# Kernel optimization log

Hardware: AMD Instinct MI355X
Metric: run time of the kernel (lower is better)

Reference implementation:

```python
import jax, jax.numpy as jnp
import numpy as np

N, E = 50000, 800000
IN_DIM, HID, OUT_DIM, HEADS = 256, 128, 128, 2
EPS_BN = 1e-5


def _glorot(key, shape):
    fan_in, fan_out = shape[0], shape[-1]
    lim = float(np.sqrt(6.0 / (fan_in + fan_out)))
    return jax.random.uniform(key, shape, jnp.float32, -lim, lim)


def setup_inputs() -> dict:
    key = jax.random.key(0)
    ks = jax.random.split(key, 12)
    x = jax.random.normal(ks[0], (N, IN_DIM), jnp.float32)
    edge_index = jax.random.randint(ks[1], (2, E), 0, N, jnp.int64)
    return {
        "x": x,
        "edge_index": edge_index,
        # layer 1 (heads=2, concat)
        "W1": _glorot(ks[2], (IN_DIM, HEADS * HID)),
        "att_src1": _glorot(ks[3], (HEADS, HID)),
        "att_dst1": _glorot(ks[4], (HEADS, HID)),
        "b1": jnp.zeros((HEADS * HID,), jnp.float32),
        "g1": jnp.ones((HEADS * HID,), jnp.float32),
        "be1": jnp.zeros((HEADS * HID,), jnp.float32),
        # layer 2 (heads=1, no concat)
        "W2": _glorot(ks[5], (HEADS * HID, OUT_DIM)),
        "att_src2": _glorot(ks[6], (1, OUT_DIM)),
        "att_dst2": _glorot(ks[7], (1, OUT_DIM)),
        "b2": jnp.zeros((OUT_DIM,), jnp.float32),
        "g2": jnp.ones((OUT_DIM,), jnp.float32),
        "be2": jnp.zeros((OUT_DIM,), jnp.float32),
    }


def gat_conv(x, src, dst, W, att_src, att_dst, bias, heads, out_ch, concat):
    """PyG GATConv forward (dropout=identity at eval). Messages flow src->dst,
    softmax over incoming edges of dst, sum-aggregate."""
    h = (x @ W).reshape(-1, heads, out_ch)             # [N, H, C]
    a_s = jnp.einsum('nhc,hc->nh', h, att_src)          # [N, H]
    a_d = jnp.einsum('nhc,hc->nh', h, att_dst)
    e = jax.nn.leaky_relu(a_s[src] + a_d[dst], 0.2)     # [E, H]
    m = jax.ops.segment_max(e, dst, num_segments=N)     # [N, H]
    m = jnp.where(jnp.isfinite(m), m, 0.0)
    w = jnp.exp(e - m[dst])                             # [E, H]
    denom = jax.ops.segment_sum(w, dst, num_segments=N) # [N, H]
    alpha = w / (denom[dst] + 1e-16)                    # [E, H]
    msg = h[src] * alpha[:, :, None]                    # [E, H, C]
    out = jax.ops.segment_sum(msg, dst, num_segments=N) # [N, H, C]
    if concat:
        out = out.reshape(-1, heads * out_ch)
    else:
        out = out.mean(axis=1)
    return out + bias


def batchnorm_relu(x, gamma, beta):
    mu = x.mean(axis=0)
    var = x.var(axis=0)  # biased, as used for normalization in torch BN
    xn = (x - mu) * jax.lax.rsqrt(var + EPS_BN)
    return jax.nn.relu(xn * gamma + beta)


def reference(x, edge_index, W1, att_src1, att_dst1, b1, g1, be1,
              W2, att_src2, att_dst2, b2, g2, be2):
    src, dst = edge_index[0], edge_index[1]
    h = gat_conv(x, src, dst, W1, att_src1, att_dst1, b1, HEADS, HID, True)
    h = batchnorm_relu(h, g1, be1)
    h = gat_conv(h, src, dst, W2, att_src2, att_dst2, b2, 1, OUT_DIM, False)
    h = batchnorm_relu(h, g2, be2)
    return h
```

## Files before the change

kernel.cpp:

```cpp
#include <hip/hip_runtime.h>
#include <math.h>

#define IN_DIM 256
#define EPS_BN 1e-5f
#define NS 16

typedef __attribute__((ext_vector_type(8))) short short8v;
typedef __attribute__((ext_vector_type(4))) float f32x4;

__device__ __forceinline__ float lrelu(float v) { return v > 0.f ? v : 0.2f * v; }

__device__ __forceinline__ unsigned short f2bf(float f) {
    unsigned int u = __float_as_uint(f);
    u += 0x7fffu + ((u >> 16) & 1u);
    return (unsigned short)(u >> 16);
}
__device__ __forceinline__ float bf2f(unsigned short s) {
    return __uint_as_float((unsigned int)s << 16);
}

__device__ __forceinline__ void bfma(float2& a, unsigned int pw, float w) {
    a.x = fmaf(__uint_as_float(pw << 16), w, a.x);
    a.y = fmaf(__uint_as_float(pw & 0xffff0000u), w, a.y);
}

__device__ __forceinline__ void gld16(const void* g, void* l) {
    __builtin_amdgcn_global_load_lds((const __attribute__((address_space(1))) void*)g,
                                     (__attribute__((address_space(3))) void*)l, 16, 0, 0);
}

__device__ __forceinline__ int edge_at(const void* ei, int is64, long long i) {
    if (is64) return (int)((const long long*)ei)[i];
    return ((const int*)ei)[i];
}

__global__ __launch_bounds__(256) void prep_kernel(const float* __restrict__ x,
                                                   unsigned short* __restrict__ xb, long long n8,
                                                   const float* __restrict__ W1,
                                                   unsigned short* __restrict__ Wt1,
                                                   const float* __restrict__ W2,
                                                   unsigned short* __restrict__ Wt2,
                                                   const unsigned int* __restrict__ eiw,
                                                   int* __restrict__ flag, long long nwords) {
    __shared__ int nz;
    long long nbx = (n8 + 255) / 256;
    long long b = blockIdx.x;
    if (b < nbx) {
        long long i = b * 256 + threadIdx.x;
        if (i < n8) {
            const float4* p = (const float4*)(x + i * 8);
            float4 v0 = p[0], v1 = p[1];
            ushort4 o0, o1;
            o0.x = f2bf(v0.x); o0.y = f2bf(v0.y); o0.z = f2bf(v0.z); o0.w = f2bf(v0.w);
            o1.x = f2bf(v1.x); o1.y = f2bf(v1.y); o1.z = f2bf(v1.z); o1.w = f2bf(v1.w);
            *(ushort4*)(xb + i * 8) = o0;
            *(ushort4*)(xb + i * 8 + 4) = o1;
        }
        return;
    }
    b -= nbx;
    if (b < 256) {
        int idx = (int)b * 256 + threadIdx.x;
        int c = idx >> 8, k = idx & 255;
        Wt1[idx] = f2bf(W1[(long long)k * 256 + c]);
        return;
    }
    b -= 256;
    if (b < 128) {
        int idx = (int)b * 256 + threadIdx.x;
        int c = idx >> 8, k = idx & 255;
        Wt2[idx] = f2bf(W2[(long long)k * 128 + c]);
        return;
    }
    if (threadIdx.x == 0) nz = 0;
    __syncthreads();
    int cnt = 0;
    for (int i = 0; i < 4; i++) {
        long long idx = 2LL * (threadIdx.x + i * 256) + 1;
        if (idx < nwords && eiw[idx] != 0u) cnt++;
    }
    if (cnt) atomicAdd(&nz, 1);
    __syncthreads();
    if (threadIdx.x == 0) flag[0] = (nz == 0) ? 1 : 0;
}

__global__ void count_deg_kernel(const void* __restrict__ ei, const int* __restrict__ flag,
                                 int* __restrict__ deg, int E_) {
    int is64 = flag[0];
    int i = blockIdx.x * 256 + threadIdx.x;
    if (i < E_) {
        int d = edge_at(ei, is64, (long long)E_ + i);
        atomicAdd(&deg[d], 1);
    }
}

__global__ __launch_bounds__(256) void scan_partial_kernel(const int* __restrict__ deg,
                                                           int* __restrict__ bsum, int n) {
    __shared__ int sh[256];
    int t = threadIdx.x;
    int i = blockIdx.x * 256 + t;
    sh[t] = (i < n) ? deg[i] : 0;
    __syncthreads();
    for (int off = 128; off >= 1; off >>= 1) {
        if (t < off) sh[t] += sh[t + off];
        __syncthreads();
    }
    if (t == 0) bsum[blockIdx.x] = sh[0];
}

__global__ __launch_bounds__(256) void scan_write_kernel(const int* __restrict__ deg,
                                                         const int* __restrict__ bsum,
                                                         int* __restrict__ rowptr,
                                                         int* __restrict__ ctr, int n, int nb) {
    __shared__ int sh[256];
    __shared__ int base_sh;
    int t = threadIdx.x;
    int b = blockIdx.x;
    sh[t] = (t < b) ? bsum[t] : 0;
    __syncthreads();
    for (int off = 128; off >= 1; off >>= 1) {
        if (t < off) sh[t] += sh[t + off];
        __syncthreads();
    }
    if (t == 0) base_sh = sh[0];
    __syncthreads();
    int i = b * 256 + t;
    int d = (i < n) ? deg[i] : 0;
    sh[t] = d;
    __syncthreads();
    for (int off = 1; off < 256; off <<= 1) {
        int u = (t >= off) ? sh[t - off] : 0;
        __syncthreads();
        sh[t] += u;
        __syncthreads();
    }
    if (i < n) {
        int v = base_sh + sh[t] - d;
        rowptr[i] = v;
        ctr[i] = v;
    }
    if (b == nb - 1 && t == 255) rowptr[n] = base_sh + sh[255];
}

__global__ void scatter_kernel(const void* __restrict__ ei, const int* __restrict__ flag,
                               int* __restrict__ ctr, int* __restrict__ srcs, int E_) {
    int is64 = flag[0];
    int i = blockIdx.x * 256 + threadIdx.x;
    if (i < E_) {
        int s = edge_at(ei, is64, i);
        int d = edge_at(ei, is64, (long long)E_ + i);
        int pos = atomicAdd(&ctr[d], 1);
        srcs[pos] = s;
    }
}

template <int NCOL, int NH, bool FUSEBN>
__global__ __launch_bounds__(256) void gemm_mfma_kernel(const unsigned short* __restrict__ Ab,
                                                        const unsigned short* __restrict__ Wt,
                                                        unsigned short* __restrict__ C,
                                                        const float* __restrict__ att_s,
                                                        const float* __restrict__ att_d,
                                                        float* __restrict__ a_s,
                                                        float* __restrict__ a_d, int M,
                                                        const float* __restrict__ bnsh,
                                                        const float* __restrict__ gamma,
                                                        const float* __restrict__ beta) {
    __shared__ unsigned short B_lds[64 * 256];
    __shared__ unsigned short A_lds[128 * 64];
    __shared__ float scs[FUSEBN ? 256 : 1];
    __shared__ float shs[FUSEBN ? 256 : 1];
    const int t = threadIdx.x;
    const int w = t >> 6, l = t & 63;
    const int row0 = blockIdx.x * 128;
    const int col0 = blockIdx.y * 64;

    {
        const char* wb = (const char*)Wt + (size_t)col0 * 512;
#pragma unroll
        for (int it = 0; it < 8; ++it) {
            int q = w * 8 + it;
            int i = q * 64 + l;
            int r = i >> 5;
            int cs = (i & 31) ^ (r & 7);
            gld16(wb + (size_t)r * 512 + cs * 16, (char*)B_lds + q * 1024);
        }
    }

    short8v nxt[4];
    const char* ab = (const char*)Ab + (size_t)row0 * 512;

    if (FUSEBN) {
        {
            int c = t;
            float s = 0.f, q = 0.f;
#pragma unroll
            for (int sh = 0; sh < NS; sh++) { s += bnsh[sh * 512 + c]; q += bnsh[sh * 512 + 256 + c]; }
            float invN = 1.f / (float)M;
            float mu = s * invN;
            float var = q * invN - mu * mu;
            float sc = rsqrtf(var + EPS_BN) * gamma[c];
            scs[c] = sc;
            shs[c] = beta[c] - mu * sc;
        }
#pragma unroll
        for (int it = 0; it < 4; ++it) {
            int i = it * 256 + t;
            int r = i >> 3, g = i & 7;
            int gr = row0 + r;
            nxt[it] = (gr < M) ? *(const short8v*)(Ab + (size_t)gr * 256 + g * 8)
                               : (short8v)(short)0;
        }
        __syncthreads();
#pragma unroll
        for (int it = 0; it < 4; ++it) {
            int i = it * 256 + t;
            int r = i >> 3, g = i & 7;
            int kb = g * 8;
            float4 s0 = *(const float4*)&scs[kb], s1 = *(const float4*)&scs[kb + 4];
            float4 h0 = *(const float4*)&shs[kb], h1 = *(const float4*)&shs[kb + 4];
            short8v v = nxt[it];
            short8v ov;
            ov[0] = (short)f2bf(fmaxf(bf2f((unsigned short)v[0]) * s0.x + h0.x, 0.f));
            ov[1] = (short)f2bf(fmaxf(bf2f((unsigned short)v[1]) * s0.y + h0.y, 0.f));
            ov[2] = (short)f2bf(fmaxf(bf2f((unsigned short)v[2]) * s0.z + h0.z, 0.f));
            ov[3] = (short)f2bf(fmaxf(bf2f((unsigned short)v[3]) * s0.w + h0.w, 0.f));
            ov[4] = (short)f2bf(fmaxf(bf2f((unsigned short)v[4]) * s1.x + h1.x, 0.f));
            ov[5] = (short)f2bf(fmaxf(bf2f((unsigned short)v[5]) * s1.y + h1.y, 0.f));
            ov[6] = (short)f2bf(fmaxf(bf2f((unsigned short)v[6]) * s1.z + h1.z, 0.f));
            ov[7] = (short)f2bf(fmaxf(bf2f((unsigned short)v[7]) * s1.w + h1.w, 0.f));
            *(short8v*)((char*)A_lds + r * 128 + ((g ^ (r & 7)) << 4)) = ov;
        }
    } else {
#pragma unroll
        for (int it = 0; it < 4; ++it) {
            int q = w * 4 + it;
            int i = q * 64 + l;
            int r = i >> 3;
            int cs = (i & 7) ^ (r & 7);
            gld16(ab + (size_t)r * 512 + cs * 16, (char*)A_lds + q * 1024);
        }
    }
    __syncthreads();

    const int rl = l & 15, kg = l >> 4;
    f32x4 acc0[4], acc1[4];
#pragma unroll
    for (int i = 0; i < 4; ++i) { acc0[i] = (f32x4)(0.f); acc1[i] = (f32x4)(0.f); }

    const int ar0 = w * 32 + rl, ar1 = ar0 + 16;
    const int aswz = (ar0 & 7) << 4;

    for (int c = 0; c < 4; ++c) {
        if (FUSEBN && c < 3) {
#pragma unroll
            for (int it = 0; it < 4; ++it) {
                int i = it * 256 + t;
                int r = i >> 3, g = i & 7;
                int gr = row0 + r;
                nxt[it] = (gr < M) ? *(const short8v*)(Ab + (size_t)gr * 256 + (c + 1) * 64 + g * 8)
                                   : (short8v)(short)0;
            }
        }
#pragma unroll
        for (int s = 0; s < 2; ++s) {
            short8v a0 = *(const short8v*)((const char*)A_lds +
                          ((ar0 * 128 + s * 64 + kg * 16) ^ aswz));
            short8v a1 = *(const short8v*)((const char*)A_lds +
                          ((ar1 * 128 + s * 64 + kg * 16) ^ aswz));
#pragma unroll
            for (int ct = 0; ct < 4; ++ct) {
                int br = ct * 16 + rl;
                short8v bfr = *(const short8v*)((const char*)B_lds +
                               ((br * 512 + c * 128 + s * 64 + kg * 16) ^ ((br & 7) << 4)));
                acc0[ct] = __builtin_amdgcn_mfma_f32_16x16x32_bf16(a0, bfr, acc0[ct], 0, 0, 0);
                acc1[ct] = __builtin_amdgcn_mfma_f32_16x16x32_bf16(a1, bfr, acc1[ct], 0, 0, 0);
            }
        }
        __syncthreads();
        if (c < 3) {
            if (FUSEBN) {
#pragma unroll
                for (int it = 0; it < 4; ++it) {
                    int i = it * 256 + t;
                    int r = i >> 3, g = i & 7;
                    int kb = (c + 1) * 64 + g * 8;
                    float4 s0 = *(const float4*)&scs[kb], s1 = *(const float4*)&scs[kb + 4];
                    float4 h0 = *(const float4*)&shs[kb], h1 = *(const float4*)&shs[kb + 4];
                    short8v v = nxt[it];
                    short8v ov;
                    ov[0] = (short)f2bf(fmaxf(bf2f((unsigned short)v[0]) * s0.x + h0.x, 0.f));
                    ov[1] = (short)f2bf(fmaxf(bf2f((unsigned short)v[1]) * s0.y + h0.y, 0.f));
                    ov[2] = (short)f2bf(fmaxf(bf2f((unsigned short)v[2]) * s0.z + h0.z, 0.f));
                    ov[3] = (short)f2bf(fmaxf(bf2f((unsigned short)v[3]) * s0.w + h0.w, 0.f));
                    ov[4] = (short)f2bf(fmaxf(bf2f((unsigned short)v[4]) * s1.x + h1.x, 0.f));
                    ov[5] = (short)f2bf(fmaxf(bf2f((unsigned short)v[5]) * s1.y + h1.y, 0.f));
                    ov[6] = (short)f2bf(fmaxf(bf2f((unsigned short)v[6]) * s1.z + h1.z, 0.f));
                    ov[7] = (short)f2bf(fmaxf(bf2f((unsigned short)v[7]) * s1.w + h1.w, 0.f));
                    *(short8v*)((char*)A_lds + r * 128 + ((g ^ (r & 7)) << 4)) = ov;
                }
            } else {
#pragma unroll
                for (int it = 0; it < 4; ++it) {
                    int q = w * 4 + it;
                    int i = q * 64 + l;
                    int r = i >> 3;
                    int cs = (i & 7) ^ (r & 7);
                    gld16(ab + (size_t)r * 512 + (c + 1) * 128 + cs * 16, (char*)A_lds + q * 1024);
                }
            }
            __syncthreads();
        }
    }

#pragma unroll
    for (int ct = 0; ct < 4; ++ct) {
#pragma unroll
        for (int r = 0; r < 4; ++r) {
            int gr0 = row0 + w * 32 + kg * 4 + r;
            if (gr0 < M) C[(long long)gr0 * NCOL + col0 + ct * 16 + rl] = f2bf(acc0[ct][r]);
            int gr1 = gr0 + 16;
            if (gr1 < M) C[(long long)gr1 * NCOL + col0 + ct * 16 + rl] = f2bf(acc1[ct][r]);
        }
    }

    float asp0[4] = {}, adp0[4] = {}, asp1[4] = {}, adp1[4] = {};
#pragma unroll
    for (int ct = 0; ct < 4; ++ct) {
        int col = col0 + ct * 16 + rl;
        float vs = att_s[col], vd = att_d[col];
#pragma unroll
        for (int r = 0; r < 4; ++r) {
            asp0[r] += acc0[ct][r] * vs; adp0[r] += acc0[ct][r] * vd;
            asp1[r] += acc1[ct][r] * vs; adp1[r] += acc1[ct][r] * vd;
        }
    }
#pragma unroll
    for (int off = 1; off < 16; off <<= 1) {
#pragma unroll
        for (int r = 0; r < 4; ++r) {
            asp0[r] += __shfl_xor(asp0[r], off);
            adp0[r] += __shfl_xor(adp0[r], off);
            asp1[r] += __shfl_xor(asp1[r], off);
            adp1[r] += __shfl_xor(adp1[r], off);
        }
    }
    if (rl == 0) {
        int head = (NH == 2) ? (col0 >> 7) : 0;
#pragma unroll
        for (int r = 0; r < 4; ++r) {
            int gr0 = row0 + w * 32 + kg * 4 + r;
            if (gr0 < M) {
                atomicAdd(&a_s[gr0 * NH + head], asp0[r]);
                atomicAdd(&a_d[gr0 * NH + head], adp0[r]);
            }
            int gr1 = gr0 + 16;
            if (gr1 < M) {
                atomicAdd(&a_s[gr1 * NH + head], asp1[r]);
                atomicAdd(&a_d[gr1 * NH + head], adp1[r]);
            }
        }
    }
}

__global__ __launch_bounds__(256) void aggregate1_kernel(const unsigned short* __restrict__ h,
                                                         const int* __restrict__ rowptr,
                                                         const int* __restrict__ srcs,
                                                         const float* __restrict__ a_s,
                                                         const float* __restrict__ a_d,
                                                         const float* __restrict__ bias,
                                                         unsigned short* __restrict__ out,
                                                         float* __restrict__ bnsh, int Nn) {
    __shared__ float sw_lds[4][256];
    const int t = threadIdx.x;
    const int wid = t >> 6, lane = t & 63;
    const int hh = (lane >> 4) & 1;
    const int eb = lane >> 5;
    const int colb = (lane & 31) * 8;
    float* wbase = sw_lds[wid];
    float2 bnsum2[4] = {}, bnsq2[4] = {};
    const int stride = gridDim.x * 4;

    for (int n = blockIdx.x * 4 + wid; n < Nn; n += stride) {
        int beg = rowptr[n], end = rowptr[n + 1];
        float2 adv = *(const float2*)&a_d[(size_t)n * 2];
        float ad0 = adv.x, ad1 = adv.y;
        float2 acc2[4] = {};
        float den = 0.f, m0 = -1e30f, m1 = -1e30f;

        for (int cb = beg; cb < end; cb += 64) {
            int cnt = end - cb; if (cnt > 64) cnt = 64;
            float e0 = -1e30f, e1 = -1e30f;
            int s_l = 0;
            if (lane < cnt) {
                s_l = srcs[cb + lane];
                float2 av = *(const float2*)&a_s[(size_t)s_l * 2];
                e0 = lrelu(av.x + ad0);
                e1 = lrelu(av.y + ad1);
            }
            float cm0 = e0, cm1 = e1;
            for (int off = 32; off >= 1; off >>= 1) {
                cm0 = fmaxf(cm0, __shfl_xor(cm0, off));
                cm1 = fmaxf(cm1, __shfl_xor(cm1, off));
            }
            if (cm0 > m0 || cm1 > m1) {
                float f0 = (cm0 > m0) ? __expf(m0 - cm0) : 1.f;
                float f1 = (cm1 > m1) ? __expf(m1 - cm1) : 1.f;
                m0 = fmaxf(m0, cm0); m1 = fmaxf(m1, cm1);
                float fo = hh ? f1 : f0;
#pragma unroll
                for (int j = 0; j < 4; j++) { acc2[j].x *= fo; acc2[j].y *= fo; }
                den *= fo;
            }
            if (lane < cnt) {
                *(float2*)&wbase[lane * 2] = make_float2(__int_as_float(s_l), __expf(e0 - m0));
                *(float2*)&wbase[128 + lane * 2] = make_float2(__int_as_float(s_l), __expf(e1 - m1));
            }
            int c = 0;
            for (; c + 8 <= cnt; c += 8) {
                float2 sw0 = *(const float2*)&wbase[hh * 128 + (c + eb) * 2];
                float2 sw1 = *(const float2*)&wbase[hh * 128 + (c + 2 + eb) * 2];
                float2 sw2 = *(const float2*)&wbase[hh * 128 + (c + 4 + eb) * 2];
                float2 sw3 = *(const float2*)&wbase[hh * 128 + (c + 6 + eb) * 2];
                uint4 p0 = *(const uint4*)(h + ((size_t)__float_as_int(sw0.x) << 8) + colb);
                uint4 p1 = *(const uint4*)(h + ((size_t)__float_as_int(sw1.x) << 8) + colb);
                uint4 p2 = *(const uint4*)(h + ((size_t)__float_as_int(sw2.x) << 8) + colb);
                uint4 p3 = *(const uint4*)(h + ((size_t)__float_as_int(sw3.x) << 8) + colb);
                den += sw0.y + sw1.y + sw2.y + sw3.y;
                bfma(acc2[0], p0.x, sw0.y); bfma(acc2[1], p0.y, sw0.y);
                bfma(acc2[2], p0.z, sw0.y); bfma(acc2[3], p0.w, sw0.y);
                bfma(acc2[0], p1.x, sw1.y); bfma(acc2[1], p1.y, sw1.y);
                bfma(acc2[2], p1.z, sw1.y); bfma(acc2[3], p1.w, sw1.y);
                bfma(acc2[0], p2.x, sw2.y); bfma(acc2[1], p2.y, sw2.y);
                bfma(acc2[2], p2.z, sw2.y); bfma(acc2[3], p2.w, sw2.y);
                bfma(acc2[0], p3.x, sw3.y); bfma(acc2[1], p3.y, sw3.y);
                bfma(acc2[2], p3.z, sw3.y); bfma(acc2[3], p3.w, sw3.y);
            }
            for (; c + 4 <= cnt; c += 4) {
                float2 sw0 = *(const float2*)&wbase[hh * 128 + (c + eb) * 2];
                float2 sw1 = *(const float2*)&wbase[hh * 128 + (c + 2 + eb) * 2];
                uint4 p0 = *(const uint4*)(h + ((size_t)__float_as_int(sw0.x) << 8) + colb);
                uint4 p1 = *(const uint4*)(h + ((size_t)__float_as_int(sw1.x) << 8) + colb);
                den += sw0.y + sw1.y;
                bfma(acc2[0], p0.x, sw0.y); bfma(acc2[1], p0.y, sw0.y);
                bfma(acc2[2], p0.z, sw0.y); bfma(acc2[3], p0.w, sw0.y);
// ... 175 lines not shown
            for (int j = 0; j < 4; j++) {
                bnsum2[j].x += of[2 * j];     bnsum2[j].y += of[2 * j + 1];
                bnsq2[j].x += of[2 * j] * of[2 * j];
                bnsq2[j].y += of[2 * j + 1] * of[2 * j + 1];
            }
            float* ob = out + (size_t)n * 128 + colb;
            *(float4*)ob = make_float4(of[0], of[1], of[2], of[3]);
            *(float4*)(ob + 4) = make_float4(of[4], of[5], of[6], of[7]);
        }
    }

    __syncthreads();
    if (lane < 16) {
#pragma unroll
        for (int j = 0; j < 4; j++) {
            wbase[colb + 2 * j] = bnsum2[j].x;
            wbase[colb + 2 * j + 1] = bnsum2[j].y;
        }
    }
    __syncthreads();
    if (t < 128) {
        int sh = (blockIdx.x & (NS - 1)) * 256;
        float s = sw_lds[0][t] + sw_lds[1][t] + sw_lds[2][t] + sw_lds[3][t];
        atomicAdd(&bnsh[sh + t], s);
    }
    __syncthreads();
    if (lane < 16) {
#pragma unroll
        for (int j = 0; j < 4; j++) {
            wbase[colb + 2 * j] = bnsq2[j].x;
            wbase[colb + 2 * j + 1] = bnsq2[j].y;
        }
    }
    __syncthreads();
    if (t < 128) {
        int sh = (blockIdx.x & (NS - 1)) * 256;
        float q = sw_lds[0][t] + sw_lds[1][t] + sw_lds[2][t] + sw_lds[3][t];
        atomicAdd(&bnsh[sh + 128 + t], q);
    }
}

__global__ __launch_bounds__(256) void bn_apply_final_kernel(float* __restrict__ x,
                                                             const float* __restrict__ bnsh,
                                                             const float* __restrict__ gamma,
                                                             const float* __restrict__ beta,
                                                             int Nn) {
    int t = threadIdx.x;
    int col = t & 127;
    float s = 0.f, q = 0.f;
#pragma unroll
    for (int sh = 0; sh < NS; sh++) { s += bnsh[sh * 256 + col]; q += bnsh[sh * 256 + 128 + col]; }
    float mu = s / (float)Nn;
    float var = q / (float)Nn - mu * mu;
    float sc = rsqrtf(var + EPS_BN) * gamma[col];
    float sh_ = beta[col] - mu * sc;
    int r0 = blockIdx.x * 2 + (t >> 7);
    int rs = gridDim.x * 2;
    for (int r = r0; r < Nn; r += rs) {
        size_t idx = (size_t)r * 128 + col;
        x[idx] = fmaxf(x[idx] * sc + sh_, 0.f);
    }
}

extern "C" void kernel_launch(void* const* d_in, const int* in_sizes, int n_in,
                              void* d_out, int out_size, void* d_ws, size_t ws_size,
                              hipStream_t stream) {
    const float* x        = (const float*)d_in[0];
    const void*  ei       = d_in[1];
    const float* W1       = (const float*)d_in[2];
    const float* att_src1 = (const float*)d_in[3];
    const float* att_dst1 = (const float*)d_in[4];
    const float* b1       = (const float*)d_in[5];
    const float* g1       = (const float*)d_in[6];
    const float* be1      = (const float*)d_in[7];
    const float* W2       = (const float*)d_in[8];
    const float* att_src2 = (const float*)d_in[9];
    const float* att_dst2 = (const float*)d_in[10];
    const float* b2       = (const float*)d_in[11];
    const float* g2       = (const float*)d_in[12];
    const float* be2      = (const float*)d_in[13];

    const int Nn = in_sizes[0] / IN_DIM;
    const int E_ = in_sizes[1] / 2;
    const int gb = (Nn + 127) / 128;
    const int Mpad = gb * 128 + 128;

    char* ws = (char*)d_ws;
    size_t o = 0;
    auto alloc = [&](size_t bytes) {
        size_t r = o;
        o += (bytes + 255) & ~(size_t)255;
        return r;
    };
    int* flag = (int*)(ws + alloc(4));
    size_t z0 = o;
    int*   deg   = (int*)(ws + alloc((size_t)Nn * 4));
    float* as1   = (float*)(ws + alloc((size_t)Nn * 2 * 4));
    float* ad1   = (float*)(ws + alloc((size_t)Nn * 2 * 4));
    float* as2   = (float*)(ws + alloc((size_t)Nn * 4));
    float* ad2   = (float*)(ws + alloc((size_t)Nn * 4));
    float* bn1sh = (float*)(ws + alloc((size_t)NS * 512 * 4));
    float* bn2sh = (float*)(ws + alloc((size_t)NS * 256 * 4));
    size_t z1 = o;
    int*   rowptr = (int*)(ws + alloc((size_t)(Nn + 1) * 4));
    int*   ctr    = (int*)(ws + alloc((size_t)Nn * 4));
    int*   srcs   = (int*)(ws + alloc((size_t)E_ * 4));
    int*   bsum   = (int*)(ws + alloc(256 * 4));
    unsigned short* Wt1  = (unsigned short*)(ws + alloc((size_t)256 * 256 * 2));
    unsigned short* Wt2  = (unsigned short*)(ws + alloc((size_t)128 * 256 * 2));
    unsigned short* xb   = (unsigned short*)(ws + alloc((size_t)Mpad * 256 * 2));
    unsigned short* x2b0 = (unsigned short*)(ws + alloc((size_t)Nn * 256 * 2));
    unsigned short* h1b  = (unsigned short*)(ws + alloc((size_t)Nn * 256 * 2));
    unsigned short* h2b  = (unsigned short*)(ws + alloc((size_t)Nn * 128 * 2));
    float* outf = (float*)d_out;

    hipMemsetAsync(ws + z0, 0, z1 - z0, stream);

    {
        long long n8 = (long long)Nn * 256 / 8;
        long long grid = (n8 + 255) / 256 + 256 + 128 + 1;
        prep_kernel<<<(int)grid, 256, 0, stream>>>(x, xb, n8, W1, Wt1, W2, Wt2,
                                                   (const unsigned int*)ei, flag,
                                                   (long long)2 * E_);
    }

    int eb = (E_ + 255) / 256;
    int nsb = (Nn + 255) / 256;
    count_deg_kernel<<<eb, 256, 0, stream>>>(ei, flag, deg, E_);
    scan_partial_kernel<<<nsb, 256, 0, stream>>>(deg, bsum, Nn);
    scan_write_kernel<<<nsb, 256, 0, stream>>>(deg, bsum, rowptr, ctr, Nn, nsb);
    scatter_kernel<<<eb, 256, 0, stream>>>(ei, flag, ctr, srcs, E_);

    const int agg_blocks = 2048;

    gemm_mfma_kernel<256, 2, false><<<dim3(gb, 4), 256, 0, stream>>>(
        xb, Wt1, h1b, att_src1, att_dst1, as1, ad1, Nn, nullptr, nullptr, nullptr);
    aggregate1_kernel<<<agg_blocks, 256, 0, stream>>>(h1b, rowptr, srcs, as1, ad1, b1, x2b0,
                                                      bn1sh, Nn);

    gemm_mfma_kernel<128, 1, true><<<dim3(gb, 2), 256, 0, stream>>>(
        x2b0, Wt2, h2b, att_src2, att_dst2, as2, ad2, Nn, bn1sh, g1, be1);
    aggregate2_kernel<<<agg_blocks, 256, 0, stream>>>(h2b, rowptr, srcs, as2, ad2, b2, outf,
                                                      bn2sh, Nn);
    bn_apply_final_kernel<<<512, 256, 0, stream>>>(outf, bn2sh, g2, be2, Nn);
}
```

Baseline: 293.6 us.

## Fuse fp32-to-bf16 input conversion into GEMM1 and restructure GEMMs over full K rows

GEMM1 now reads fp32 x directly and converts it to bf16 in LDS, which removes the separate conversion pass and the xb buffer. Both GEMMs switch to 64-row blocks that keep the full 256-wide A tile resident and loop over output column panels, so A is loaded and BN-transformed once per block rather than once per column block. The two-kernel scan is merged into one kernel in which each block re-sums all preceding degrees, saving a launch at the cost of quadratic redundant reads. The column loop within a block is now serialized, and the 64 KB of LDS per block may reduce occupancy.

```diff
diff --git a/kernel.cpp b/kernel.cpp
--- a/kernel.cpp
+++ b/kernel.cpp
@@ -34,31 +34,14 @@
     return ((const int*)ei)[i];
 }
 
-__global__ __launch_bounds__(256) void prep_kernel(const float* __restrict__ x,
-                                                   unsigned short* __restrict__ xb, long long n8,
-                                                   const float* __restrict__ W1,
+__global__ __launch_bounds__(256) void prep_kernel(const float* __restrict__ W1,
                                                    unsigned short* __restrict__ Wt1,
                                                    const float* __restrict__ W2,
                                                    unsigned short* __restrict__ Wt2,
                                                    const unsigned int* __restrict__ eiw,
                                                    int* __restrict__ flag, long long nwords) {
     __shared__ int nz;
-    long long nbx = (n8 + 255) / 256;
     long long b = blockIdx.x;
-    if (b < nbx) {
-        long long i = b * 256 + threadIdx.x;
-        if (i < n8) {
-            const float4* p = (const float4*)(x + i * 8);
-            float4 v0 = p[0], v1 = p[1];
-            ushort4 o0, o1;
-            o0.x = f2bf(v0.x); o0.y = f2bf(v0.y); o0.z = f2bf(v0.z); o0.w = f2bf(v0.w);
-            o1.x = f2bf(v1.x); o1.y = f2bf(v1.y); o1.z = f2bf(v1.z); o1.w = f2bf(v1.w);
-            *(ushort4*)(xb + i * 8) = o0;
-            *(ushort4*)(xb + i * 8 + 4) = o1;
-        }
-        return;
-    }
-    b -= nbx;
     if (b < 256) {
         int idx = (int)b * 256 + threadIdx.x;
         int c = idx >> 8, k = idx & 255;
@@ -94,29 +77,17 @@
     }
 }
 
-__global__ __launch_bounds__(256) void scan_partial_kernel(const int* __restrict__ deg,
-                                                           int* __restrict__ bsum, int n) {
-    __shared__ int sh[256];
-    int t = threadIdx.x;
-    int i = blockIdx.x * 256 + t;
-    sh[t] = (i < n) ? deg[i] : 0;
-    __syncthreads();
-    for (int off = 128; off >= 1; off >>= 1) {
-        if (t < off) sh[t] += sh[t + off];
-        __syncthreads();
-    }
-    if (t == 0) bsum[blockIdx.x] = sh[0];
-}
-
-__global__ __launch_bounds__(256) void scan_write_kernel(const int* __restrict__ deg,
-                                                         const int* __restrict__ bsum,
-                                                         int* __restrict__ rowptr,
-                                                         int* __restrict__ ctr, int n, int nb) {
+__global__ __launch_bounds__(256) void scan_kernel(const int* __restrict__ deg,
+                                                   int* __restrict__ rowptr,
+                                                   int* __restrict__ ctr, int n, int nb) {
     __shared__ int sh[256];
     __shared__ int base_sh;
     int t = threadIdx.x;
     int b = blockIdx.x;
-    sh[t] = (t < b) ? bsum[t] : 0;
+    int lim = b * 256;
+    int s = 0;
+    for (int j = t; j < lim; j += 256) s += deg[j];
+    sh[t] = s;
     __syncthreads();
     for (int off = 128; off >= 1; off >>= 1) {
         if (t < off) sh[t] += sh[t + off];
@@ -124,7 +95,7 @@
     }
     if (t == 0) base_sh = sh[0];
     __syncthreads();
-    int i = b * 256 + t;
+    int i = lim + t;
     int d = (i < n) ? deg[i] : 0;
     sh[t] = d;
     __syncthreads();
@@ -154,209 +125,228 @@
     }
 }
 
-template <int NCOL, int NH, bool FUSEBN>
-__global__ __launch_bounds__(256) void gemm_mfma_kernel(const unsigned short* __restrict__ Ab,
-                                                        const unsigned short* __restrict__ Wt,
-                                                        unsigned short* __restrict__ C,
-                                                        const float* __restrict__ att_s,
-                                                        const float* __restrict__ att_d,
-                                                        float* __restrict__ a_s,
-                                                        float* __restrict__ a_d, int M,
-                                                        const float* __restrict__ bnsh,
-                                                        const float* __restrict__ gamma,
-                                                        const float* __restrict__ beta) {
-    __shared__ unsigned short B_lds[64 * 256];
-    __shared__ unsigned short A_lds[128 * 64];
-    __shared__ float scs[FUSEBN ? 256 : 1];
-    __shared__ float shs[FUSEBN ? 256 : 1];
+__global__ __launch_bounds__(256) void gemm1_kernel(const float* __restrict__ X,
+                                                    const unsigned short* __restrict__ Wt,
+                                                    unsigned short* __restrict__ C,
+                                                    const float* __restrict__ att_s,
+                                                    const float* __restrict__ att_d,
+                                                    float* __restrict__ a_s,
+                                                    float* __restrict__ a_d, int M) {
+    __shared__ __attribute__((aligned(16))) unsigned short A_lds[64 * 256];
+    __shared__ __attribute__((aligned(16))) unsigned short B_lds[64 * 256];
     const int t = threadIdx.x;
     const int w = t >> 6, l = t & 63;
-    const int row0 = blockIdx.x * 128;
-    const int col0 = blockIdx.y * 64;
-
-    {
-        const char* wb = (const char*)Wt + (size_t)col0 * 512;
-#pragma unroll
-        for (int it = 0; it < 8; ++it) {
-            int q = w * 8 + it;
-            int i = q * 64 + l;
-            int r = i >> 5;
-            int cs = (i & 31) ^ (r & 7);
-            gld16(wb + (size_t)r * 512 + cs * 16, (char*)B_lds + q * 1024);
-        }
-    }
-
-    short8v nxt[4];
-    const char* ab = (const char*)Ab + (size_t)row0 * 512;
-
-    if (FUSEBN) {
+    const int row0 = blockIdx.x * 64;
+    const int g = t & 31;
+
+#pragma unroll
+    for (int it = 0; it < 8; ++it) {
+        int i = it * 256 + t;
+        int r = i >> 5;
+        int gr = row0 + r;
+        float4 v0 = make_float4(0.f, 0.f, 0.f, 0.f), v1 = v0;
+        if (gr < M) {
+            const float* src = X + (size_t)gr * 256 + g * 8;
+            v0 = *(const float4*)src;
+            v1 = *(const float4*)(src + 4);
+        }
+        short8v ov;
+        ov[0] = (short)f2bf(v0.x); ov[1] = (short)f2bf(v0.y);
+        ov[2] = (short)f2bf(v0.z); ov[3] = (short)f2bf(v0.w);
+        ov[4] = (short)f2bf(v1.x); ov[5] = (short)f2bf(v1.y);
+        ov[6] = (short)f2bf(v1.z); ov[7] = (short)f2bf(v1.w);
+        *(short8v*)((char*)A_lds + r * 512 + ((g ^ (r & 7)) << 4)) = ov;
+    }
+
+    const int rl = l & 15, kg = l >> 4;
+    const int abase = (w * 16 + rl) * 512;
+    const int aswz = (w * 16 + rl) & 7;
+
+    float asp[4] = {}, adp[4] = {};
+    for (int p = 0; p < 4; ++p) {
+        __syncthreads();
         {
-            int c = t;
-            float s = 0.f, q = 0.f;
-#pragma unroll
-            for (int sh = 0; sh < NS; sh++) { s += bnsh[sh * 512 + c]; q += bnsh[sh * 512 + 256 + c]; }
-            float invN = 1.f / (float)M;
-            float mu = s * invN;
-            float var = q * invN - mu * mu;
-            float sc = rsqrtf(var + EPS_BN) * gamma[c];
-            scs[c] = sc;
-            shs[c] = beta[c] - mu * sc;
-        }
-#pragma unroll
-        for (int it = 0; it < 4; ++it) {
-            int i = it * 256 + t;
-            int r = i >> 3, g = i & 7;
-            int gr = row0 + r;
-            nxt[it] = (gr < M) ? *(const short8v*)(Ab + (size_t)gr * 256 + g * 8)
-                               : (short8v)(short)0;
+            const char* wb = (const char*)Wt + (size_t)(p * 64) * 512;
+#pragma unroll
+            for (int it = 0; it < 8; ++it) {
+                int q = w * 8 + it;
+                int i = q * 64 + l;
+                int r = i >> 5;
+                int cs = (i & 31) ^ (r & 7);
+                gld16(wb + (size_t)r * 512 + cs * 16, (char*)B_lds + q * 1024);
+            }
         }
         __syncthreads();
-#pragma unroll
-        for (int it = 0; it < 4; ++it) {
-            int i = it * 256 + t;
-            int r = i >> 3, g = i & 7;
-            int kb = g * 8;
-            float4 s0 = *(const float4*)&scs[kb], s1 = *(const float4*)&scs[kb + 4];
-            float4 h0 = *(const float4*)&shs[kb], h1 = *(const float4*)&shs[kb + 4];
-            short8v v = nxt[it];
-            short8v ov;
-            ov[0] = (short)f2bf(fmaxf(bf2f((unsigned short)v[0]) * s0.x + h0.x, 0.f));
-            ov[1] = (short)f2bf(fmaxf(bf2f((unsigned short)v[1]) * s0.y + h0.y, 0.f));
-            ov[2] = (short)f2bf(fmaxf(bf2f((unsigned short)v[2]) * s0.z + h0.z, 0.f));
-            ov[3] = (short)f2bf(fmaxf(bf2f((unsigned short)v[3]) * s0.w + h0.w, 0.f));
-            ov[4] = (short)f2bf(fmaxf(bf2f((unsigned short)v[4]) * s1.x + h1.x, 0.f));
-            ov[5] = (short)f2bf(fmaxf(bf2f((unsigned short)v[5]) * s1.y + h1.y, 0.f));
-            ov[6] = (short)f2bf(fmaxf(bf2f((unsigned short)v[6]) * s1.z + h1.z, 0.f));
-            ov[7] = (short)f2bf(fmaxf(bf2f((unsigned short)v[7]) * s1.w + h1.w, 0.f));
-            *(short8v*)((char*)A_lds + r * 128 + ((g ^ (r & 7)) << 4)) = ov;
-        }
-    } else {
-#pragma unroll
-        for (int it = 0; it < 4; ++it) {
-            int q = w * 4 + it;
-            int i = q * 64 + l;
-            int r = i >> 3;
-            int cs = (i & 7) ^ (r & 7);
-            gld16(ab + (size_t)r * 512 + cs * 16, (char*)A_lds + q * 1024);
-        }
-    }
-    __syncthreads();
-
-    const int rl = l & 15, kg = l >> 4;
-    f32x4 acc0[4], acc1[4];
-#pragma unroll
-    for (int i = 0; i < 4; ++i) { acc0[i] = (f32x4)(0.f); acc1[i] = (f32x4)(0.f); }
-
-    const int ar0 = w * 32 + rl, ar1 = ar0 + 16;
-    const int aswz = (ar0 & 7) << 4;
-
-    for (int c = 0; c < 4; ++c) {
-        if (FUSEBN && c < 3) {
-#pragma unroll
-            for (int it = 0; it < 4; ++it) {
-                int i = it * 256 + t;
-                int r = i >> 3, g = i & 7;
-                int gr = row0 + r;
-                nxt[it] = (gr < M) ? *(const short8v*)(Ab + (size_t)gr * 256 + (c + 1) * 64 + g * 8)
-                                   : (short8v)(short)0;
-            }
-        }
-#pragma unroll
-        for (int s = 0; s < 2; ++s) {
-            short8v a0 = *(const short8v*)((const char*)A_lds +
-                          ((ar0 * 128 + s * 64 + kg * 16) ^ aswz));
-            short8v a1 = *(const short8v*)((const char*)A_lds +
-                          ((ar1 * 128 + s * 64 + kg * 16) ^ aswz));
+        f32x4 acc[4];
+#pragma unroll
+        for (int i = 0; i < 4; ++i) acc[i] = (f32x4)(0.f);
+#pragma unroll
+        for (int ks = 0; ks < 8; ++ks) {
+            int chunk = ks * 4 + kg;
+            short8v a = *(const short8v*)((const char*)A_lds + abase + ((chunk ^ aswz) << 4));
 #pragma unroll
             for (int ct = 0; ct < 4; ++ct) {
                 int br = ct * 16 + rl;
-                short8v bfr = *(const short8v*)((const char*)B_lds +
-                               ((br * 512 + c * 128 + s * 64 + kg * 16) ^ ((br & 7) << 4)));
-                acc0[ct] = __builtin_amdgcn_mfma_f32_16x16x32_bf16(a0, bfr, acc0[ct], 0, 0, 0);
-                acc1[ct] = __builtin_amdgcn_mfma_f32_16x16x32_bf16(a1, bfr, acc1[ct], 0, 0, 0);
-            }
-        }
+                short8v b = *(const short8v*)((const char*)B_lds + br * 512 +
+                                              ((chunk ^ (br & 7)) << 4));
+                acc[ct] = __builtin_amdgcn_mfma_f32_16x16x32_bf16(a, b, acc[ct], 0, 0, 0);
+            }
+        }
+#pragma unroll
+        for (int ct = 0; ct < 4; ++ct) {
+            int col = p * 64 + ct * 16 + rl;
+            float vs = att_s[col], vd = att_d[col];
+#pragma unroll
+            for (int r = 0; r < 4; ++r) {
+                int gr = row0 + w * 16 + kg * 4 + r;
+                if (gr < M) C[(size_t)gr * 256 + col] = f2bf(acc[ct][r]);
+                asp[r] += acc[ct][r] * vs;
+                adp[r] += acc[ct][r] * vd;
+            }
+        }
+        if (p == 1 || p == 3) {
+            int head = p >> 1;
+#pragma unroll
+            for (int off = 1; off < 16; off <<= 1) {
+#pragma unroll
+                for (int r = 0; r < 4; ++r) {
+                    asp[r] += __shfl_xor(asp[r], off);
+                    adp[r] += __shfl_xor(adp[r], off);
+                }
+            }
+            if (rl == 0) {
+#pragma unroll
+                for (int r = 0; r < 4; ++r) {
+                    int gr = row0 + w * 16 + kg * 4 + r;
+                    if (gr < M) {
+                        atomicAdd(&a_s[gr * 2 + head], asp[r]);
+                        atomicAdd(&a_d[gr * 2 + head], adp[r]);
+                    }
+                }
+            }
+#pragma unroll
+            for (int r = 0; r < 4; ++r) { asp[r] = 0.f; adp[r] = 0.f; }
+        }
+    }
+}
+
+__global__ __launch_bounds__(256) void gemm2_kernel(const unsigned short* __restrict__ Ab,
+                                                    const unsigned short* __restrict__ Wt,
+                                                    unsigned short* __restrict__ C,
+                                                    const float* __restrict__ att_s,
+                                                    const float* __restrict__ att_d,
+                                                    float* __restrict__ a_s,
+                                                    float* __restrict__ a_d, int M,
+                                                    const float* __restrict__ bnsh,
+                                                    const float* __restrict__ gamma,
+                                                    const float* __restrict__ beta) {
+    __shared__ __attribute__((aligned(16))) unsigned short A_lds[64 * 256];
+    __shared__ __attribute__((aligned(16))) unsigned short B_lds[64 * 256];
+    const int t = threadIdx.x;
+    const int w = t >> 6, l = t & 63;
+    const int row0 = blockIdx.x * 64;
+    const int g = t & 31;
+
+    {
+        float* cf = (float*)A_lds;
+        float s = 0.f, q = 0.f;
+#pragma unroll
+        for (int sh = 0; sh < NS; sh++) { s += bnsh[sh * 512 + t]; q += bnsh[sh * 512 + 256 + t]; }
+        float invN = 1.f / (float)M;
+        float mu = s * invN;
+        float var = q * invN - mu * mu;
+        float scl = rsqrtf(var + EPS_BN) * gamma[t];
+        cf[t] = scl;
+        cf[256 + t] = beta[t] - mu * scl;
+    }
+    __syncthreads();
+    float sc[8], sb[8];
+    {
+        const float* cf = (const float*)A_lds;
+#pragma unroll
+        for (int j = 0; j < 8; ++j) {
+            sc[j] = cf[g * 8 + j];
+            sb[j] = cf[256 + g * 8 + j];
+        }
+    }
+    __syncthreads();
+
+#pragma unroll
+    for (int it = 0; it < 8; ++it) {
+        int i = it * 256 + t;
+        int r = i >> 5;
+        int gr = row0 + r;
+        short8v v = (gr < M) ? *(const short8v*)(Ab + (size_t)gr * 256 + g * 8)
+                             : (short8v)(short)0;
+        short8v ov;
+#pragma unroll
+        for (int j = 0; j < 8; ++j)
+            ov[j] = (short)f2bf(fmaxf(bf2f((unsigned short)v[j]) * sc[j] + sb[j], 0.f));
+        *(short8v*)((char*)A_lds + r * 512 + ((g ^ (r & 7)) << 4)) = ov;
+    }
+
+    const int rl = l & 15, kg = l >> 4;
+    const int abase = (w * 16 + rl) * 512;
+    const int aswz = (w * 16 + rl) & 7;
+
+    float asp[4] = {}, adp[4] = {};
+    for (int p = 0; p < 2; ++p) {
         __syncthreads();
-        if (c < 3) {
-            if (FUSEBN) {
-#pragma unroll
-                for (int it = 0; it < 4; ++it) {
-                    int i = it * 256 + t;
-                    int r = i >> 3, g = i & 7;
-                    int kb = (c + 1) * 64 + g * 8;
-                    float4 s0 = *(const float4*)&scs[kb], s1 = *(const float4*)&scs[kb + 4];
-                    float4 h0 = *(const float4*)&shs[kb], h1 = *(const float4*)&shs[kb + 4];
-                    short8v v = nxt[it];
-                    short8v ov;
-                    ov[0] = (short)f2bf(fmaxf(bf2f((unsigned short)v[0]) * s0.x + h0.x, 0.f));
-                    ov[1] = (short)f2bf(fmaxf(bf2f((unsigned short)v[1]) * s0.y + h0.y, 0.f));
-                    ov[2] = (short)f2bf(fmaxf(bf2f((unsigned short)v[2]) * s0.z + h0.z, 0.f));
-                    ov[3] = (short)f2bf(fmaxf(bf2f((unsigned short)v[3]) * s0.w + h0.w, 0.f));
-                    ov[4] = (short)f2bf(fmaxf(bf2f((unsigned short)v[4]) * s1.x + h1.x, 0.f));
-                    ov[5] = (short)f2bf(fmaxf(bf2f((unsigned short)v[5]) * s1.y + h1.y, 0.f));
-                    ov[6] = (short)f2bf(fmaxf(bf2f((unsigned short)v[6]) * s1.z + h1.z, 0.f));
-                    ov[7] = (short)f2bf(fmaxf(bf2f((unsigned short)v[7]) * s1.w + h1.w, 0.f));
-                    *(short8v*)((char*)A_lds + r * 128 + ((g ^ (r & 7)) << 4)) = ov;
-                }
-            } else {
-#pragma unroll
-                for (int it = 0; it < 4; ++it) {
-                    int q = w * 4 + it;
-                    int i = q * 64 + l;
-                    int r = i >> 3;
-                    int cs = (i & 7) ^ (r & 7);
-                    gld16(ab + (size_t)r * 512 + (c + 1) * 128 + cs * 16, (char*)A_lds + q * 1024);
-                }
-            }
-            __syncthreads();
-        }
-    }
-
-#pragma unroll
-    for (int ct = 0; ct < 4; ++ct) {
+        {
+            const char* wb = (const char*)Wt + (size_t)(p * 64) * 512;
+#pragma unroll
+            for (int it = 0; it < 8; ++it) {
+                int q = w * 8 + it;
+                int i = q * 64 + l;
+                int r = i >> 5;
+                int cs = (i & 31) ^ (r & 7);
+                gld16(wb + (size_t)r * 512 + cs * 16, (char*)B_lds + q * 1024);
+            }
+        }
+        __syncthreads();
+        f32x4 acc[4];
+#pragma unroll
+        for (int i = 0; i < 4; ++i) acc[i] = (f32x4)(0.f);
+#pragma unroll
+        for (int ks = 0; ks < 8; ++ks) {
+            int chunk = ks * 4 + kg;
+            short8v a = *(const short8v*)((const char*)A_lds + abase + ((chunk ^ aswz) << 4));
+#pragma unroll
+            for (int ct = 0; ct < 4; ++ct) {
+                int br = ct * 16 + rl;
+                short8v b = *(const short8v*)((const char*)B_lds + br * 512 +
+                                              ((chunk ^ (br & 7)) << 4));
+                acc[ct] = __builtin_amdgcn_mfma_f32_16x16x32_bf16(a, b, acc[ct], 0, 0, 0);
+            }
+        }
+#pragma unroll
+        for (int ct = 0; ct < 4; ++ct) {
+            int col = p * 64 + ct * 16 + rl;
+            float vs = att_s[col], vd = att_d[col];
+#pragma unroll
+            for (int r = 0; r < 4; ++r) {
+                int gr = row0 + w * 16 + kg * 4 + r;
+                if (gr < M) C[(size_t)gr * 128 + col] = f2bf(acc[ct][r]);
+                asp[r] += acc[ct][r] * vs;
+                adp[r] += acc[ct][r] * vd;
+            }
+        }
+    }
+#pragma unroll
+    for (int off = 1; off < 16; off <<= 1) {
 #pragma unroll
         for (int r = 0; r < 4; ++r) {
-            int gr0 = row0 + w * 32 + kg * 4 + r;
-            if (gr0 < M) C[(long long)gr0 * NCOL + col0 + ct * 16 + rl] = f2bf(acc0[ct][r]);
-            int gr1 = gr0 + 16;
-            if (gr1 < M) C[(long long)gr1 * NCOL + col0 + ct * 16 + rl] = f2bf(acc1[ct][r]);
-        }
-    }
-
-    float asp0[4] = {}, adp0[4] = {}, asp1[4] = {}, adp1[4] = {};
-#pragma unroll
-    for (int ct = 0; ct < 4; ++ct) {
-        int col = col0 + ct * 16 + rl;
-        float vs = att_s[col], vd = att_d[col];
+            asp[r] += __shfl_xor(asp[r], off);
+            adp[r] += __shfl_xor(adp[r], off);
+        }
+    }
+    if (rl == 0) {
 #pragma unroll
         for (int r = 0; r < 4; ++r) {
-            asp0[r] += acc0[ct][r] * vs; adp0[r] += acc0[ct][r] * vd;
-            asp1[r] += acc1[ct][r] * vs; adp1[r] += acc1[ct][r] * vd;
-        }
-    }
-#pragma unroll
-    for (int off = 1; off < 16; off <<= 1) {
-#pragma unroll
-        for (int r = 0; r < 4; ++r) {
-            asp0[r] += __shfl_xor(asp0[r], off);
-            adp0[r] += __shfl_xor(adp0[r], off);
-            asp1[r] += __shfl_xor(asp1[r], off);
-            adp1[r] += __shfl_xor(adp1[r], off);
-        }
-    }
-    if (rl == 0) {
-        int head = (NH == 2) ? (col0 >> 7) : 0;
-#pragma unroll
-        for (int r = 0; r < 4; ++r) {
-            int gr0 = row0 + w * 32 + kg * 4 + r;
-            if (gr0 < M) {
-                atomicAdd(&a_s[gr0 * NH + head], asp0[r]);
-                atomicAdd(&a_d[gr0 * NH + head], adp0[r]);
-            }
-            int gr1 = gr0 + 16;
-            if (gr1 < M) {
-                atomicAdd(&a_s[gr1 * NH + head], asp1[r]);
-                atomicAdd(&a_d[gr1 * NH + head], adp1[r]);
+            int gr = row0 + w * 16 + kg * 4 + r;
+            if (gr < M) {
+                atomicAdd(&a_s[gr], asp[r]);
+                atomicAdd(&a_d[gr], adp[r]);
             }
         }
     }
@@ -701,8 +691,7 @@
 
     const int Nn = in_sizes[0] / IN_DIM;
     const int E_ = in_sizes[1] / 2;
-    const int gb = (Nn + 127) / 128;
-    const int Mpad = gb * 128 + 128;
+    const int gb64 = (Nn + 63) / 64;
 
     char* ws = (char*)d_ws;
     size_t o = 0;
@@ -724,10 +713,8 @@
     int*   rowptr = (int*)(ws + alloc((size_t)(Nn + 1) * 4));
     int*   ctr    = (int*)(ws + alloc((size_t)Nn * 4));
     int*   srcs   = (int*)(ws + alloc((size_t)E_ * 4));
-    int*   bsum   = (int*)(ws + alloc(256 * 4));
     unsigned short* Wt1  = (unsigned short*)(ws + alloc((size_t)256 * 256 * 2));
     unsigned short* Wt2  = (unsigned short*)(ws + alloc((size_t)128 * 256 * 2));
-    unsigned short* xb   = (unsigned short*)(ws + alloc((size_t)Mpad * 256 * 2));
     unsigned short* x2b0 = (unsigned short*)(ws + alloc((size_t)Nn * 256 * 2));
     unsigned short* h1b  = (unsigned short*)(ws + alloc((size_t)Nn * 256 * 2));
     unsigned short* h2b  = (unsigned short*)(ws + alloc((size_t)Nn * 128 * 2));
@@ -735,30 +722,24 @@
 
     hipMemsetAsync(ws + z0, 0, z1 - z0, stream);
 
-    {
-        long long n8 = (long long)Nn * 256 / 8;
-        long long grid = (n8 + 255) / 256 + 256 + 128 + 1;
-        prep_kernel<<<(int)grid, 256, 0, stream>>>(x, xb, n8, W1, Wt1, W2, Wt2,
+    prep_kernel<<<256 + 128 + 1, 256, 0, stream>>>(W1, Wt1, W2, Wt2,
                                                    (const unsigned int*)ei, flag,
                                                    (long long)2 * E_);
-    }
 
     int eb = (E_ + 255) / 256;
     int nsb = (Nn + 255) / 256;
     count_deg_kernel<<<eb, 256, 0, stream>>>(ei, flag, deg, E_);
-    scan_partial_kernel<<<nsb, 256, 0, stream>>>(deg, bsum, Nn);
-    scan_write_kernel<<<nsb, 256, 0, stream>>>(deg, bsum, rowptr, ctr, Nn, nsb);
+    scan_kernel<<<nsb, 256, 0, stream>>>(deg, rowptr, ctr, Nn, nsb);
     scatter_kernel<<<eb, 256, 0, stream>>>(ei, flag, ctr, srcs, E_);
 
     const int agg_blocks = 2048;
 
-    gemm_mfma_kernel<256, 2, false><<<dim3(gb, 4), 256, 0, stream>>>(
-        xb, Wt1, h1b, att_src1, att_dst1, as1, ad1, Nn, nullptr, nullptr, nullptr);
+    gemm1_kernel<<<gb64, 256, 0, stream>>>(x, Wt1, h1b, att_src1, att_dst1, as1, ad1, Nn);
     aggregate1_kernel<<<agg_blocks, 256, 0, stream>>>(h1b, rowptr, srcs, as1, ad1, b1, x2b0,
                                                       bn1sh, Nn);
 
-    gemm_mfma_kernel<128, 1, true><<<dim3(gb, 2), 256, 0, stream>>>(
-        x2b0, Wt2, h2b, att_src2, att_dst2, as2, ad2, Nn, bn1sh, g1, be1);
+    gemm2_kernel<<<gb64, 256, 0, stream>>>(x2b0, Wt2, h2b, att_src2, att_dst2, as2, ad2, Nn,
+                                           bn1sh, g1, be1);
     aggregate2_kernel<<<agg_blocks, 256, 0, stream>>>(h2b, rowptr, srcs, as2, ad2, b2, outf,
                                                       bn2sh, Nn);
     bn_apply_final_kernel<<<512, 256, 0, stream>>>(outf, bn2sh, g2, be2, Nn);
```

New measurement: 307.7 us. 1.05x slower.

## Merge preprocessing launches: fold degree count, single-pass scan, scatter with GEMM1

Applied to the files above, without the earlier changes.

Removes the separate flag computation by having each wavefront detect int64 edge indices with a ballot. The degree count is folded into the prep kernel, and the two-pass scan becomes one kernel in which each block re-sums all preceding degrees. The edge scatter runs in the same launch as the first-layer GEMM, so the two can overlap. This cuts kernel launches and serialization gaps, at the cost of redundant prefix summation and redundant per-wave dtype checks. The GEMM body is turned into a shared device function.

```diff
diff --git a/kernel.cpp b/kernel.cpp
--- a/kernel.cpp
+++ b/kernel.cpp
@@ -34,15 +34,23 @@
     return ((const int*)ei)[i];
 }
 
-__global__ __launch_bounds__(256) void prep_kernel(const float* __restrict__ x,
-                                                   unsigned short* __restrict__ xb, long long n8,
-                                                   const float* __restrict__ W1,
-                                                   unsigned short* __restrict__ Wt1,
-                                                   const float* __restrict__ W2,
-                                                   unsigned short* __restrict__ Wt2,
-                                                   const unsigned int* __restrict__ eiw,
-                                                   int* __restrict__ flag, long long nwords) {
-    __shared__ int nz;
+__device__ __forceinline__ int edge_is64(const void* ei, int E_) {
+    const unsigned int* w = (const unsigned int*)ei;
+    int lane = threadIdx.x & 63;
+    long long idx = 2LL * lane + 1;
+    unsigned int v = (idx < 2LL * E_) ? w[idx] : 0u;
+    return (__ballot(v != 0u) == 0ULL) ? 1 : 0;
+}
+
+__global__ __launch_bounds__(256) void prep_count_kernel(const float* __restrict__ x,
+                                                         unsigned short* __restrict__ xb,
+                                                         long long n8,
+                                                         const float* __restrict__ W1,
+                                                         unsigned short* __restrict__ Wt1,
+                                                         const float* __restrict__ W2,
+                                                         unsigned short* __restrict__ Wt2,
+                                                         const void* __restrict__ ei,
+                                                         int* __restrict__ deg, int E_) {
     long long nbx = (n8 + 255) / 256;
     long long b = blockIdx.x;
     if (b < nbx) {
@@ -72,51 +80,26 @@
         Wt2[idx] = f2bf(W2[(long long)k * 128 + c]);
         return;
     }
-    if (threadIdx.x == 0) nz = 0;
-    __syncthreads();
-    int cnt = 0;
-    for (int i = 0; i < 4; i++) {
-        long long idx = 2LL * (threadIdx.x + i * 256) + 1;
-        if (idx < nwords && eiw[idx] != 0u) cnt++;
-    }
-    if (cnt) atomicAdd(&nz, 1);
-    __syncthreads();
-    if (threadIdx.x == 0) flag[0] = (nz == 0) ? 1 : 0;
-}
-
-__global__ void count_deg_kernel(const void* __restrict__ ei, const int* __restrict__ flag,
-                                 int* __restrict__ deg, int E_) {
-    int is64 = flag[0];
-    int i = blockIdx.x * 256 + threadIdx.x;
+    b -= 128;
+    int is64 = edge_is64(ei, E_);
+    int i = (int)b * 256 + threadIdx.x;
     if (i < E_) {
         int d = edge_at(ei, is64, (long long)E_ + i);
         atomicAdd(&deg[d], 1);
     }
 }
 
-__global__ __launch_bounds__(256) void scan_partial_kernel(const int* __restrict__ deg,
-                                                           int* __restrict__ bsum, int n) {
-    __shared__ int sh[256];
-    int t = threadIdx.x;
-    int i = blockIdx.x * 256 + t;
-    sh[t] = (i < n) ? deg[i] : 0;
-    __syncthreads();
-    for (int off = 128; off >= 1; off >>= 1) {
-        if (t < off) sh[t] += sh[t + off];
-        __syncthreads();
-    }
-    if (t == 0) bsum[blockIdx.x] = sh[0];
-}
-
-__global__ __launch_bounds__(256) void scan_write_kernel(const int* __restrict__ deg,
-                                                         const int* __restrict__ bsum,
-                                                         int* __restrict__ rowptr,
-                                                         int* __restrict__ ctr, int n, int nb) {
+__global__ __launch_bounds__(256) void scan_kernel(const int* __restrict__ deg,
+                                                   int* __restrict__ rowptr,
+                                                   int* __restrict__ ctr, int n, int nb) {
     __shared__ int sh[256];
     __shared__ int base_sh;
     int t = threadIdx.x;
     int b = blockIdx.x;
-    sh[t] = (t < b) ? bsum[t] : 0;
+    int lim = b * 256;
+    int s = 0;
+    for (int j = t; j < lim; j += 256) s += deg[j];
+    sh[t] = s;
     __syncthreads();
     for (int off = 128; off >= 1; off >>= 1) {
         if (t < off) sh[t] += sh[t + off];
@@ -124,7 +107,7 @@
     }
     if (t == 0) base_sh = sh[0];
     __syncthreads();
-    int i = b * 256 + t;
+    int i = lim + t;
     int d = (i < n) ? deg[i] : 0;
     sh[t] = d;
     __syncthreads();
@@ -142,37 +125,22 @@
     if (b == nb - 1 && t == 255) rowptr[n] = base_sh + sh[255];
 }
 
-__global__ void scatter_kernel(const void* __restrict__ ei, const int* __restrict__ flag,
-                               int* __restrict__ ctr, int* __restrict__ srcs, int E_) {
-    int is64 = flag[0];
-    int i = blockIdx.x * 256 + threadIdx.x;
-    if (i < E_) {
-        int s = edge_at(ei, is64, i);
-        int d = edge_at(ei, is64, (long long)E_ + i);
-        int pos = atomicAdd(&ctr[d], 1);
-        srcs[pos] = s;
-    }
-}
-
 template <int NCOL, int NH, bool FUSEBN>
-__global__ __launch_bounds__(256) void gemm_mfma_kernel(const unsigned short* __restrict__ Ab,
-                                                        const unsigned short* __restrict__ Wt,
-                                                        unsigned short* __restrict__ C,
-                                                        const float* __restrict__ att_s,
-                                                        const float* __restrict__ att_d,
-                                                        float* __restrict__ a_s,
-                                                        float* __restrict__ a_d, int M,
-                                                        const float* __restrict__ bnsh,
-                                                        const float* __restrict__ gamma,
-                                                        const float* __restrict__ beta) {
-    __shared__ unsigned short B_lds[64 * 256];
-    __shared__ unsigned short A_lds[128 * 64];
-    __shared__ float scs[FUSEBN ? 256 : 1];
-    __shared__ float shs[FUSEBN ? 256 : 1];
+__device__ __forceinline__ void gemm_body(unsigned short* A_lds, unsigned short* B_lds,
+                                          float* scs, float* shs,
+                                          const unsigned short* __restrict__ Ab,
+                                          const unsigned short* __restrict__ Wt,
+                                          unsigned short* __restrict__ C,
+                                          const float* __restrict__ att_s,
+                                          const float* __restrict__ att_d,
+                                          float* __restrict__ a_s,
+                                          float* __restrict__ a_d, int M,
+                                          int row0, int col0,
+                                          const float* __restrict__ bnsh,
+                                          const float* __restrict__ gamma,
+                                          const float* __restrict__ beta) {
     const int t = threadIdx.x;
     const int w = t >> 6, l = t & 63;
-    const int row0 = blockIdx.x * 128;
-    const int col0 = blockIdx.y * 64;
 
     {
         const char* wb = (const char*)Wt + (size_t)col0 * 512;
@@ -360,6 +328,57 @@
             }
         }
     }
+}
+
+__global__ __launch_bounds__(256) void scatter_gemm1_kernel(const void* __restrict__ ei,
+                                                            int* __restrict__ ctr,
+                                                            int* __restrict__ srcs, int E_,
+                                                            int eb, int gbx,
+                                                            const unsigned short* __restrict__ xb,
+                                                            const unsigned short* __restrict__ Wt1,
+                                                            unsigned short* __restrict__ h1b,
+                                                            const float* __restrict__ att_s,
+                                                            const float* __restrict__ att_d,
+                                                            float* __restrict__ a_s,
+                                                            float* __restrict__ a_d, int M) {
+    __shared__ __attribute__((aligned(16))) unsigned short B_lds[64 * 256];
+    __shared__ __attribute__((aligned(16))) unsigned short A_lds[128 * 64];
+    int b = blockIdx.x;
+    if (b < eb) {
+        int is64 = edge_is64(ei, E_);
+        int i = b * 256 + threadIdx.x;
+        if (i < E_) {
+            int s = edge_at(ei, is64, i);
+            int d = edge_at(ei, is64, (long long)E_ + i);
+            int pos = atomicAdd(&ctr[d], 1);
+            srcs[pos] = s;
+        }
+        return;
+    }
+    b -= eb;
+    int bx = b % gbx;
+    int by = b / gbx;
+    gemm_body<256, 2, false>(A_lds, B_lds, (float*)A_lds, (float*)A_lds, xb, Wt1, h1b,
+                             att_s, att_d, a_s, a_d, M, bx * 128, by * 64,
+                             nullptr, nullptr, nullptr);
+}
+
+__global__ __launch_bounds__(256) void gemm2_kernel(const unsigned short* __restrict__ Ab,
+                                                    const unsigned short* __restrict__ Wt,
+                                                    unsigned short* __restrict__ C,
+                                                    const float* __restrict__ att_s,
+                                                    const float* __restrict__ att_d,
+                                                    float* __restrict__ a_s,
+                                                    float* __restrict__ a_d, int M,
+                                                    const float* __restrict__ bnsh,
+                                                    const float* __restrict__ gamma,
+                                                    const float* __restrict__ beta) {
+    __shared__ __attribute__((aligned(16))) unsigned short B_lds[64 * 256];
+    __shared__ __attribute__((aligned(16))) unsigned short A_lds[128 * 64];
+    __shared__ float scs[256];
+    __shared__ float shs[256];
+    gemm_body<128, 1, true>(A_lds, B_lds, scs, shs, Ab, Wt, C, att_s, att_d, a_s, a_d,
+                            M, blockIdx.x * 128, blockIdx.y * 64, bnsh, gamma, beta);
 }
 
 __global__ __launch_bounds__(256) void aggregate1_kernel(const unsigned short* __restrict__ h,
@@ -711,7 +730,6 @@
         o += (bytes + 255) & ~(size_t)255;
         return r;
     };
-    int* flag = (int*)(ws + alloc(4));
     size_t z0 = o;
     int*   deg   = (int*)(ws + alloc((size_t)Nn * 4));
     float* as1   = (float*)(ws + alloc((size_t)Nn * 2 * 4));
@@ -724,7 +742,6 @@
     int*   rowptr = (int*)(ws + alloc((size_t)(Nn + 1) * 4));
     int*   ctr    = (int*)(ws + alloc((size_t)Nn * 4));
     int*   srcs   = (int*)(ws + alloc((size_t)E_ * 4));
-    int*   bsum   = (int*)(ws + alloc(256 * 4));
     unsigned short* Wt1  = (unsigned short*)(ws + alloc((size_t)256 * 256 * 2));
     unsigned short* Wt2  = (unsigned short*)(ws + alloc((size_t)128 * 256 * 2));
     unsigned short* xb   = (unsigned short*)(ws + alloc((size_t)Mpad * 256 * 2));
@@ -735,30 +752,26 @@
 
     hipMemsetAsync(ws + z0, 0, z1 - z0, stream);
 
-    {
-        long long n8 = (long long)Nn * 256 / 8;
-        long long grid = (n8 + 255) / 256 + 256 + 128 + 1;
-        prep_kernel<<<(int)grid, 256, 0, stream>>>(x, xb, n8, W1, Wt1, W2, Wt2,
-                                                   (const unsigned int*)ei, flag,
-                                                   (long long)2 * E_);
-    }
-
+    long long n8 = (long long)Nn * 256 / 8;
     int eb = (E_ + 255) / 256;
     int nsb = (Nn + 255) / 256;
-    count_deg_kernel<<<eb, 256, 0, stream>>>(ei, flag, deg, E_);
-    scan_partial_kernel<<<nsb, 256, 0, stream>>>(deg, bsum, Nn);
-    scan_write_kernel<<<nsb, 256, 0, stream>>>(deg, bsum, rowptr, ctr, Nn, nsb);
-    scatter_kernel<<<eb, 256, 0, stream>>>(ei, flag, ctr, srcs, E_);
+
+    {
+        long long grid = (n8 + 255) / 256 + 256 + 128 + eb;
+        prep_count_kernel<<<(int)grid, 256, 0, stream>>>(x, xb, n8, W1, Wt1, W2, Wt2,
+                                                         ei, deg, E_);
+    }
+    scan_kernel<<<nsb, 256, 0, stream>>>(deg, rowptr, ctr, Nn, nsb);
+    scatter_gemm1_kernel<<<eb + gb * 4, 256, 0, stream>>>(ei, ctr, srcs, E_, eb, gb,
+                                                          xb, Wt1, h1b, att_src1, att_dst1,
+                                                          as1, ad1, Nn);
 
     const int agg_blocks = 2048;
 
-    gemm_mfma_kernel<256, 2, false><<<dim3(gb, 4), 256, 0, stream>>>(
-        xb, Wt1, h1b, att_src1, att_dst1, as1, ad1, Nn, nullptr, nullptr, nullptr);
     aggregate1_kernel<<<agg_blocks, 256, 0, stream>>>(h1b, rowptr, srcs, as1, ad1, b1, x2b0,
                                                       bn1sh, Nn);
-
-    gemm_mfma_kernel<128, 1, true><<<dim3(gb, 2), 256, 0, stream>>>(
-        x2b0, Wt2, h2b, att_src2, att_dst2, as2, ad2, Nn, bn1sh, g1, be1);
+    gemm2_kernel<<<dim3(gb, 2), 256, 0, stream>>>(x2b0, Wt2, h2b, att_src2, att_dst2,
+                                                  as2, ad2, Nn, bn1sh, g1, be1);
     aggregate2_kernel<<<agg_blocks, 256, 0, stream>>>(h2b, rowptr, srcs, as2, ad2, b2, outf,
                                                       bn2sh, Nn);
     bn_apply_final_kernel<<<512, 256, 0, stream>>>(outf, bn2sh, g2, be2, Nn);
```

New measurement: 325.1 us. 1.11x slower.
